# Performance work log

Measured on AMD Instinct MI355X. Metric: run time of the kernel, lower is better.

The kernel has to match this reference:

```python
import jax, jax.numpy as jnp
import numpy as np

B, N, C, T, K = 32, 4096, 768, 1000, 20

def setup_inputs() -> dict:
    key = jax.random.key(0)
    k1, k2, k3, k4 = jax.random.split(key, 4)
    g_feat = jax.random.normal(k1, (B, 1, C), dtype=jnp.float32)
    inp = jax.random.normal(k2, (B, N, C), dtype=jnp.float32)
    tau = jax.random.uniform(k3, (1,), dtype=jnp.float32)
    text_embeddings = jax.random.normal(k4, (T, C), dtype=jnp.float32) * 0.01
    return {"g_feat": g_feat, "input": inp, "tau": tau, "text_embeddings": text_embeddings}


def reference(g_feat, input, tau, text_embeddings):
    feat = input  # [B, N, C]
    # 1x1 conv of global feature against text embeddings -> class logits [B, T]
    vg_logit = jnp.einsum('bc,tc->bt', g_feat[:, 0, :], text_embeddings)
    # top-20 candidate categories per image
    _, indices = jax.lax.top_k(vg_logit, K)              # [B, K]
    agg_text_features = text_embeddings[indices]          # [B, K, C] gather
    # per-pixel logits against the 20 gathered text embeddings
    seg_logit = jnp.exp(tau[0]) * jnp.einsum('bkc,bnc->bkn', agg_text_features, feat)  # [B, K, N]
    # hard (straight-through) softmax over candidate axis (dim=-2)
    y_soft = jax.nn.softmax(seg_logit, axis=-2)
    idx = jnp.argmax(seg_logit, axis=-2)                  # [B, N]
    y_hard = jnp.moveaxis(jax.nn.one_hot(idx, K, dtype=seg_logit.dtype), -1, -2)  # [B, K, N]
    attn = y_hard - jax.lax.stop_gradient(y_soft) + y_soft
    # normalize over pixel axis (assign_eps = 1.0)
    assign_attn = attn / (jnp.sum(attn, axis=-1, keepdims=True) + 1.0)
    # combine: [B, N, K] @ [B, K, C] -> [B, N, C]
    text_grids = jnp.einsum('bkn,bkc->bnc', assign_attn, agg_text_features)
    return text_grids
```

## Files before the change

### kernel.cpp

```cpp
#include <hip/hip_runtime.h>
#include <cfloat>

#define B_ 32
#define N_ 4096
#define C_ 768
#define T_ 1000
#define K_ 20

#define PXB 256
#define PHC 16
#define NPH (C_/PHC)
#define GAP_TH 1e-3f
#define MAXF 16384

typedef float f32x4 __attribute__((ext_vector_type(4)));

__global__ __launch_bounds__(256) void k1_logits(const float* __restrict__ g_feat,
                                                 const float* __restrict__ text,
                                                 double* __restrict__ logits,
                                                 int* __restrict__ cnt,
                                                 int* __restrict__ flagcnt) {
    int b = blockIdx.x;
    int wid = threadIdx.x >> 6, lane = threadIdx.x & 63;
    int t = blockIdx.y * 4 + wid;
    if (b == 0 && blockIdx.y == 0) {
        for (int i = threadIdx.x; i < B_ * K_; i += 256) cnt[i] = 0;
        if (threadIdx.x == 0) flagcnt[0] = 0;
    }
    const float* g = g_feat + b * C_;
    const float* e = text + t * C_;
    double s = 0.0;
    #pragma unroll
    for (int j = 0; j < 12; ++j) {
        int c = lane + 64 * j;
        s += (double)g[c] * (double)e[c];
    }
    #pragma unroll
    for (int m = 32; m; m >>= 1) s += __shfl_xor(s, m);
    if (lane == 0) logits[b * T_ + t] = s;
}

__global__ __launch_bounds__(256) void k1b_topk(const double* __restrict__ logits,
                                                const float* __restrict__ text,
                                                float* __restrict__ agg,
                                                int* __restrict__ sel) {
    __shared__ int ssel[K_];
    int b = blockIdx.x, tid = threadIdx.x, lane = tid & 63;
    if (tid < 64) {
        double v[16];
        #pragma unroll
        for (int j = 0; j < 16; ++j) {
            int t = lane + 64 * j;
            v[j] = (t < T_) ? logits[b * T_ + t] : -DBL_MAX;
        }
        for (int it = 0; it < K_; ++it) {
            double bv = -DBL_MAX; int bi = 0x7fffffff;
            #pragma unroll
            for (int j = 0; j < 16; ++j) {
                int t = lane + 64 * j;
                if (v[j] > bv) { bv = v[j]; bi = t; }
            }
            #pragma unroll
            for (int m = 32; m; m >>= 1) {
                double ov = __shfl_xor(bv, m); int oi = __shfl_xor(bi, m);
                if (ov > bv || (ov == bv && oi < bi)) { bv = ov; bi = oi; }
            }
            if (lane == 0) ssel[it] = bi;
            #pragma unroll
            for (int j = 0; j < 16; ++j) {
                int t = lane + 64 * j;
                if (t == bi) v[j] = -DBL_MAX;
            }
        }
    }
    __syncthreads();
    if (tid < K_) sel[b * K_ + tid] = ssel[tid];
    for (int i = tid; i < K_ * C_; i += 256) {
        int j = i / C_, c = i - j * C_;
        agg[b * K_ * C_ + i] = text[ssel[j] * C_ + c];
    }
}

__global__ __launch_bounds__(128) void k2_argmax(const float* __restrict__ feat,
                                                 const float* __restrict__ agg,
                                                 int* __restrict__ kidx,
                                                 int* __restrict__ cnt,
                                                 int* __restrict__ flagcnt,
                                                 int* __restrict__ flaglist) {
    __shared__ float fbuf[3][PXB * PHC];
    __shared__ float ebuf[3][512];
    __shared__ int scnt[K_];
    int bx = blockIdx.x;
    int b = bx >> 4, tile = bx & 15;
    int n0 = tile * PXB;
    int tid = threadIdx.x, wid = tid >> 6, lane = tid & 63;
    if (tid < K_) scnt[tid] = 0;
    __syncthreads();

    const float* fb = feat + ((size_t)b * N_ + n0) * C_;
    const float* eb = agg + b * (K_ * C_);

    int se = wid * 64 + lane;
    int ce = se < 80 ? se : 79;
    const float* esrc = eb + (ce >> 2) * C_ + (ce & 3) * 4;

    auto stage = [&](int p, int bufi) {
        #pragma unroll
        for (int ii = 0; ii < 8; ++ii) {
            int s = (wid * 8 + ii) * 64 + lane;
            int c = s ^ ((s >> 3) & 7);
            int px = c >> 2, j = c & 3;
            const float* g = fb + (size_t)px * C_ + p * PHC + j * 4;
            float* d = &fbuf[bufi][(wid * 8 + ii) * 256];
            __builtin_amdgcn_global_load_lds((const __attribute__((address_space(1))) void*)g,
                                             (__attribute__((address_space(3))) void*)d, 16, 0, 0);
        }
        {
            const float* g = esrc + p * PHC;
            float* d = &ebuf[bufi][wid * 256];
            __builtin_amdgcn_global_load_lds((const __attribute__((address_space(1))) void*)g,
                                             (__attribute__((address_space(3))) void*)d, 16, 0, 0);
        }
    };

    float acc0[K_], acc1[K_];
    #pragma unroll
    for (int k = 0; k < K_; ++k) { acc0[k] = 0.f; acc1[k] = 0.f; }

    stage(0, 0);
    stage(1, 1);

    int p0 = tid, p1 = tid + 128;
    #pragma unroll 1
    for (int p = 0; p < NPH; ++p) {
        int bufi = p % 3;
        if (p + 2 < NPH) {
            stage(p + 2, (p + 2) % 3);
            asm volatile("s_waitcnt vmcnt(18)" ::: "memory");
        } else if (p + 1 < NPH) {
            asm volatile("s_waitcnt vmcnt(9)" ::: "memory");
        } else {
            asm volatile("s_waitcnt vmcnt(0)" ::: "memory");
        }
        asm volatile("s_barrier" ::: "memory");

        const float* fB = fbuf[bufi];
        const float* eB = ebuf[bufi];
        f32x4 F0[4], F1[4];
        #pragma unroll
        for (int j = 0; j < 4; ++j) {
            int c0 = p0 * 4 + j, h0 = c0 ^ ((c0 >> 3) & 7);
            F0[j] = *(const f32x4*)(fB + h0 * 4);
            int c1 = p1 * 4 + j, h1 = c1 ^ ((c1 >> 3) & 7);
            F1[j] = *(const f32x4*)(fB + h1 * 4);
        }
        #pragma unroll
        for (int k = 0; k < K_; ++k) {
            float a0 = acc0[k], a1 = acc1[k];
            #pragma unroll
            for (int j = 0; j < 4; ++j) {
                f32x4 e = *(const f32x4*)(eB + (k * 4 + j) * 4);
                a0 = fmaf(F0[j].x, e.x, a0); a0 = fmaf(F0[j].y, e.y, a0);
                a0 = fmaf(F0[j].z, e.z, a0); a0 = fmaf(F0[j].w, e.w, a0);
                a1 = fmaf(F1[j].x, e.x, a1); a1 = fmaf(F1[j].y, e.y, a1);
                a1 = fmaf(F1[j].z, e.z, a1); a1 = fmaf(F1[j].w, e.w, a1);
            }
            acc0[k] = a0; acc1[k] = a1;
        }
        asm volatile("s_barrier" ::: "memory");
    }

    #pragma unroll
    for (int q = 0; q < 2; ++q) {
        float* acc = q ? acc1 : acc0;
        float m1 = acc[0]; int i1 = 0; float m2 = -FLT_MAX;
        #pragma unroll
        for (int k = 1; k < K_; ++k) {
            float v = acc[k];
            if (v > m1) { m2 = m1; m1 = v; i1 = k; }
            else if (v > m2) m2 = v;
        }
        int n = n0 + tid + q * 128;
        kidx[b * N_ + n] = i1;
        atomicAdd(&scnt[i1], 1);
        if (m1 - m2 < GAP_TH) {
            int pos = atomicAdd(flagcnt, 1);
            if (pos < MAXF) flaglist[pos] = b * N_ + n;
        }
    }
    __syncthreads();
    if (tid < K_) atomicAdd(&cnt[b * K_ + tid], scnt[tid]);
}

__global__ __launch_bounds__(256) void k25_refine(const float* __restrict__ feat,
                                                  const float* __restrict__ agg,
                                                  int* __restrict__ kidx,
                                                  int* __restrict__ cnt,
                                                  const int* __restrict__ flagcnt,
                                                  const int* __restrict__ flaglist) {
    int wid = threadIdx.x >> 6, lane = threadIdx.x & 63;
    int wg = blockIdx.x * 4 + wid;
    int nf = flagcnt[0]; if (nf > MAXF) nf = MAXF;
    for (int e = wg; e < nf; e += gridDim.x * 4) {
        int pix = flaglist[e];
        int b = pix >> 12;
        const float* fr = feat + (size_t)pix * C_;
        const float* ebase = agg + b * K_ * C_;
        double fd[12];
        #pragma unroll
        for (int j = 0; j < 12; ++j) fd[j] = (double)fr[lane + 64 * j];
        double best = -DBL_MAX; int bi = 0;
        for (int k = 0; k < K_; ++k) {
            const float* er = ebase + k * C_;
            double s = 0.0;
            #pragma unroll
            for (int j = 0; j < 12; ++j) s += fd[j] * (double)er[lane + 64 * j];
            #pragma unroll
            for (int m = 32; m; m >>= 1) s += __shfl_xor(s, m);
            if (s > best) { best = s; bi = k; }
        }
        if (lane == 0) {
            int old = kidx[pix];
            if (old != bi) {
                kidx[pix] = bi;
                atomicSub(&cnt[b * K_ + old], 1);
                atomicAdd(&cnt[b * K_ + bi], 1);
            }
        }
    }
}

__global__ __launch_bounds__(256) void k4_out(const float* __restrict__ agg,
                                              const int* __restrict__ cnt,
                                              const int* __restrict__ kidx,
                                              float* __restrict__ out) {
    int wid = threadIdx.x >> 6, lane = threadIdx.x & 63;
    int wg = blockIdx.x * 4 + wid;
    int base = wg * 8;
    int b = base >> 12;
    int kk[8];
    #pragma unroll
    for (int i = 0; i < 8; ++i) kk[i] = kidx[base + i];
    float sc[8];
    #pragma unroll
    for (int i = 0; i < 8; ++i) sc[i] = 1.0f / ((float)cnt[b * K_ + kk[i]] + 1.0f);
    const f32x4* agg4 = (const f32x4*)agg;
    f32x4* out4 = (f32x4*)out;
    #pragma unroll
    for (int i = 0; i < 8; ++i) {
        const f32x4* a4 = agg4 + (size_t)(b * K_ + kk[i]) * (C_ / 4);
        f32x4* o4 = out4 + (size_t)(base + i) * (C_ / 4);
        #pragma unroll
        for (int j = 0; j < 3; ++j) {
            f32x4 v = a4[lane + 64 * j];
            v *= sc[i];
            __builtin_nontemporal_store(v, &o4[lane + 64 * j]);
        }
    }
}

extern "C" void kernel_launch(void* const* d_in, const int* in_sizes, int n_in,
                              void* d_out, int out_size, void* d_ws, size_t ws_size,
                              hipStream_t stream) {
    const float* g_feat = (const float*)d_in[0];
    const float* feat   = (const float*)d_in[1];
    const float* text   = (const float*)d_in[3];
    float* out = (float*)d_out;

    char* ws = (char*)d_ws;
    double* logits = (double*)(ws + 0);
    float*  agg    = (float*) (ws + 262144);
    int*    sel    = (int*)   (ws + 2228224);
    int*    cnt    = (int*)   (ws + 2230784);
    int*    flagc  = (int*)   (ws + 2233344);
    int*    flagl  = (int*)   (ws + 2233408);
    int*    kidx   = (int*)   (ws + 2301504);

    k1_logits<<<dim3(32, 250), 256, 0, stream>>>(g_feat, text, logits, cnt, flagc);
    k1b_topk<<<32, 256, 0, stream>>>(logits, text, agg, sel);
    k2_argmax<<<32 * 16, 128, 0, stream>>>(feat, agg, kidx, cnt, flagc, flagl);
    k25_refine<<<64, 256, 0, stream>>>(feat, agg, kidx, cnt, flagc, flagl);
    k4_out<<<4096, 256, 0, stream>>>(agg, cnt, kidx, out);
}
```

Before: 299.6 us.

## Compute per-pixel logits with split-bf16 MFMA instead of fp32 FMA

Replaces the scalar fp32 FMA dot product in the argmax kernel with MFMA 16x16x32 bf16 instructions. Each fp32 operand is split into a hi and a lo bf16 part, and three cross products are accumulated to keep near-fp32 accuracy. Features are loaded into registers, converted and written to swizzled LDS; the text embeddings are pre-split into bf16 hi/lo tables in the top-k kernel. It also lowers the gap threshold for the fp32 refine pass, widens the refine grid and switches the output stores from nontemporal to regular. The risk is borderline argmax mismatches if the split-bf16 error exceeds the tighter threshold.

```diff
diff --git a/kernel.cpp b/kernel.cpp
--- a/kernel.cpp
+++ b/kernel.cpp
@@ -8,12 +8,19 @@
 #define K_ 20
 
 #define PXB 256
-#define PHC 16
+#define PHC 32
 #define NPH (C_/PHC)
-#define GAP_TH 1e-3f
+#define GAP_TH 1e-4f
 #define MAXF 16384
 
 typedef float f32x4 __attribute__((ext_vector_type(4)));
+typedef int   i32x4 __attribute__((ext_vector_type(4)));
+typedef short s16x8 __attribute__((ext_vector_type(8)));
+
+__device__ __forceinline__ unsigned short bf_rne(float x) {
+    unsigned u = __float_as_uint(x);
+    return (unsigned short)((u + 0x7fffu + ((u >> 16) & 1u)) >> 16);
+}
 
 __global__ __launch_bounds__(256) void k1_logits(const float* __restrict__ g_feat,
                                                  const float* __restrict__ text,
@@ -43,7 +50,8 @@
 __global__ __launch_bounds__(256) void k1b_topk(const double* __restrict__ logits,
                                                 const float* __restrict__ text,
                                                 float* __restrict__ agg,
-                                                int* __restrict__ sel) {
+                                                unsigned short* __restrict__ Ehi,
+                                                unsigned short* __restrict__ Elo) {
     __shared__ int ssel[K_];
     int b = blockIdx.x, tid = threadIdx.x, lane = tid & 63;
     if (tid < 64) {
@@ -74,21 +82,29 @@
         }
     }
     __syncthreads();
-    if (tid < K_) sel[b * K_ + tid] = ssel[tid];
     for (int i = tid; i < K_ * C_; i += 256) {
         int j = i / C_, c = i - j * C_;
         agg[b * K_ * C_ + i] = text[ssel[j] * C_ + c];
     }
-}
-
-__global__ __launch_bounds__(128) void k2_argmax(const float* __restrict__ feat,
-                                                 const float* __restrict__ agg,
-                                                 int* __restrict__ kidx,
-                                                 int* __restrict__ cnt,
-                                                 int* __restrict__ flagcnt,
-                                                 int* __restrict__ flaglist) {
-    __shared__ float fbuf[3][PXB * PHC];
-    __shared__ float ebuf[3][512];
+    for (int i = tid; i < 32 * C_; i += 256) {
+        int r = i / C_, c = i - r * C_;
+        float v = (r < K_) ? text[ssel[r] * C_ + c] : 0.f;
+        unsigned u = __float_as_uint(v);
+        float fh = __uint_as_float(u & 0xffff0000u);
+        Ehi[(size_t)b * 32 * C_ + i] = (unsigned short)(u >> 16);
+        Elo[(size_t)b * 32 * C_ + i] = bf_rne(v - fh);
+    }
+}
+
+__global__ __launch_bounds__(256, 2) void k2_argmax(const float* __restrict__ feat,
+                                                    const unsigned short* __restrict__ Ehi,
+                                                    const unsigned short* __restrict__ Elo,
+                                                    int* __restrict__ kidx,
+                                                    int* __restrict__ cnt,
+                                                    int* __restrict__ flagcnt,
+                                                    int* __restrict__ flaglist) {
+    __shared__ unsigned short hiT[2][PXB * PHC];
+    __shared__ unsigned short loT[2][PXB * PHC];
     __shared__ int scnt[K_];
     int bx = blockIdx.x;
     int b = bx >> 4, tile = bx & 15;
@@ -98,94 +114,120 @@
     __syncthreads();
 
     const float* fb = feat + ((size_t)b * N_ + n0) * C_;
-    const float* eb = agg + b * (K_ * C_);
-
-    int se = wid * 64 + lane;
-    int ce = se < 80 ? se : 79;
-    const float* esrc = eb + (ce >> 2) * C_ + (ce & 3) * 4;
-
-    auto stage = [&](int p, int bufi) {
-        #pragma unroll
-        for (int ii = 0; ii < 8; ++ii) {
-            int s = (wid * 8 + ii) * 64 + lane;
-            int c = s ^ ((s >> 3) & 7);
-            int px = c >> 2, j = c & 3;
-            const float* g = fb + (size_t)px * C_ + p * PHC + j * 4;
-            float* d = &fbuf[bufi][(wid * 8 + ii) * 256];
-            __builtin_amdgcn_global_load_lds((const __attribute__((address_space(1))) void*)g,
-                                             (__attribute__((address_space(3))) void*)d, 16, 0, 0);
-        }
-        {
-            const float* g = esrc + p * PHC;
-            float* d = &ebuf[bufi][wid * 256];
-            __builtin_amdgcn_global_load_lds((const __attribute__((address_space(1))) void*)g,
-                                             (__attribute__((address_space(3))) void*)d, 16, 0, 0);
-        }
+    const unsigned short* Eh = Ehi + (size_t)b * 32 * C_;
+    const unsigned short* El = Elo + (size_t)b * 32 * C_;
+    int r2 = (tid >> 1) & 3;
+    int arow = lane & 15, acg = lane >> 4;
+
+    f32x4 fr[8];
+    auto LOADF = [&](int p) {
+        const f32x4* fp_ = (const f32x4*)(fb + (size_t)tid * C_ + p * PHC);
+        #pragma unroll
+        for (int q = 0; q < 8; ++q) fr[q] = fp_[q ^ (2 * r2)];
     };
-
-    float acc0[K_], acc1[K_];
-    #pragma unroll
-    for (int k = 0; k < K_; ++k) { acc0[k] = 0.f; acc1[k] = 0.f; }
-
-    stage(0, 0);
-    stage(1, 1);
-
-    int p0 = tid, p1 = tid + 128;
+    auto CVTW = [&](int buf) {
+        #pragma unroll
+        for (int j = 0; j < 4; ++j) {
+            unsigned hu[8], lu[8];
+            #pragma unroll
+            for (int m = 0; m < 8; ++m) {
+                float x = (m < 4) ? fr[2 * j][m] : fr[2 * j + 1][m - 4];
+                unsigned u = __float_as_uint(x);
+                float fh = __uint_as_float(u & 0xffff0000u);
+                hu[m] = u >> 16;
+                lu[m] = bf_rne(x - fh);
+            }
+            int slot = tid * 4 + (j ^ r2);
+            i32x4 hv = { (int)(hu[0] | (hu[1] << 16)), (int)(hu[2] | (hu[3] << 16)),
+                         (int)(hu[4] | (hu[5] << 16)), (int)(hu[6] | (hu[7] << 16)) };
+            i32x4 lv = { (int)(lu[0] | (lu[1] << 16)), (int)(lu[2] | (lu[3] << 16)),
+                         (int)(lu[4] | (lu[5] << 16)), (int)(lu[6] | (lu[7] << 16)) };
+            *(i32x4*)&hiT[buf][slot * 8] = hv;
+            *(i32x4*)&loT[buf][slot * 8] = lv;
+        }
+    };
+
+    s16x8 Ach0, Ach1, Acl0, Acl1, Anh0, Anh1, Anl0, Anl1;
+    auto LOADA = [&](int p, s16x8& h0, s16x8& h1, s16x8& l0, s16x8& l1) {
+        int co = p * PHC + acg * 8;
+        h0 = *(const s16x8*)(Eh + (size_t)arow * C_ + co);
+        h1 = *(const s16x8*)(Eh + (size_t)(16 + arow) * C_ + co);
+        l0 = *(const s16x8*)(El + (size_t)arow * C_ + co);
+        l1 = *(const s16x8*)(El + (size_t)(16 + arow) * C_ + co);
+    };
+
+    f32x4 acc0[4], acc1[4];
+    #pragma unroll
+    for (int i = 0; i < 4; ++i) { acc0[i] = (f32x4)0.f; acc1[i] = (f32x4)0.f; }
+
+    LOADF(0);
+    CVTW(0);
+    LOADF(1);
+    LOADA(0, Ach0, Ach1, Acl0, Acl1);
+    LOADA(1, Anh0, Anh1, Anl0, Anl1);
+    __syncthreads();
+
     #pragma unroll 1
     for (int p = 0; p < NPH; ++p) {
-        int bufi = p % 3;
-        if (p + 2 < NPH) {
-            stage(p + 2, (p + 2) % 3);
-            asm volatile("s_waitcnt vmcnt(18)" ::: "memory");
-        } else if (p + 1 < NPH) {
-            asm volatile("s_waitcnt vmcnt(9)" ::: "memory");
-        } else {
-            asm volatile("s_waitcnt vmcnt(0)" ::: "memory");
+        int cur = p & 1;
+        if (p + 1 < NPH) {
+            CVTW(cur ^ 1);
+            if (p + 2 < NPH) LOADF(p + 2);
+            asm volatile("s_waitcnt lgkmcnt(0)" ::: "memory");
         }
         asm volatile("s_barrier" ::: "memory");
 
-        const float* fB = fbuf[bufi];
-        const float* eB = ebuf[bufi];
-        f32x4 F0[4], F1[4];
-        #pragma unroll
-        for (int j = 0; j < 4; ++j) {
-            int c0 = p0 * 4 + j, h0 = c0 ^ ((c0 >> 3) & 7);
-            F0[j] = *(const f32x4*)(fB + h0 * 4);
-            int c1 = p1 * 4 + j, h1 = c1 ^ ((c1 >> 3) & 7);
-            F1[j] = *(const f32x4*)(fB + h1 * 4);
-        }
-        #pragma unroll
-        for (int k = 0; k < K_; ++k) {
-            float a0 = acc0[k], a1 = acc1[k];
-            #pragma unroll
-            for (int j = 0; j < 4; ++j) {
-                f32x4 e = *(const f32x4*)(eB + (k * 4 + j) * 4);
-                a0 = fmaf(F0[j].x, e.x, a0); a0 = fmaf(F0[j].y, e.y, a0);
-                a0 = fmaf(F0[j].z, e.z, a0); a0 = fmaf(F0[j].w, e.w, a0);
-                a1 = fmaf(F1[j].x, e.x, a1); a1 = fmaf(F1[j].y, e.y, a1);
-                a1 = fmaf(F1[j].z, e.z, a1); a1 = fmaf(F1[j].w, e.w, a1);
-            }
-            acc0[k] = a0; acc1[k] = a1;
+        #pragma unroll
+        for (int i = 0; i < 4; ++i) {
+            int slot = (wid * 64 + i * 16 + arow) * 4 + acg;
+            s16x8 Bh = *(const s16x8*)&hiT[cur][slot * 8];
+            s16x8 Bl = *(const s16x8*)&loT[cur][slot * 8];
+            acc0[i] = __builtin_amdgcn_mfma_f32_16x16x32_bf16(Ach0, Bh, acc0[i], 0, 0, 0);
+            acc1[i] = __builtin_amdgcn_mfma_f32_16x16x32_bf16(Ach1, Bh, acc1[i], 0, 0, 0);
+            acc0[i] = __builtin_amdgcn_mfma_f32_16x16x32_bf16(Ach0, Bl, acc0[i], 0, 0, 0);
+            acc1[i] = __builtin_amdgcn_mfma_f32_16x16x32_bf16(Ach1, Bl, acc1[i], 0, 0, 0);
+            acc0[i] = __builtin_amdgcn_mfma_f32_16x16x32_bf16(Acl0, Bh, acc0[i], 0, 0, 0);
+            acc1[i] = __builtin_amdgcn_mfma_f32_16x16x32_bf16(Acl1, Bh, acc1[i], 0, 0, 0);
         }
         asm volatile("s_barrier" ::: "memory");
-    }
-
-    #pragma unroll
-    for (int q = 0; q < 2; ++q) {
-        float* acc = q ? acc1 : acc0;
-        float m1 = acc[0]; int i1 = 0; float m2 = -FLT_MAX;
-        #pragma unroll
-        for (int k = 1; k < K_; ++k) {
-            float v = acc[k];
-            if (v > m1) { m2 = m1; m1 = v; i1 = k; }
+
+        Ach0 = Anh0; Ach1 = Anh1; Acl0 = Anl0; Acl1 = Anl1;
+        if (p + 2 < NPH) LOADA(p + 2, Anh0, Anh1, Anl0, Anl1);
+    }
+
+    #pragma unroll
+    for (int i = 0; i < 4; ++i) {
+        int kb = acg * 4;
+        float m1 = acc0[i][0]; int i1 = kb; float m2 = -FLT_MAX;
+        #pragma unroll
+        for (int r = 1; r < 4; ++r) {
+            float v = acc0[i][r];
+            if (v > m1) { m2 = m1; m1 = v; i1 = kb + r; }
             else if (v > m2) m2 = v;
         }
-        int n = n0 + tid + q * 128;
-        kidx[b * N_ + n] = i1;
-        atomicAdd(&scnt[i1], 1);
-        if (m1 - m2 < GAP_TH) {
-            int pos = atomicAdd(flagcnt, 1);
-            if (pos < MAXF) flaglist[pos] = b * N_ + n;
+        if (acg == 0) {
+            #pragma unroll
+            for (int r = 0; r < 4; ++r) {
+                float v = acc1[i][r];
+                if (v > m1) { m2 = m1; m1 = v; i1 = 16 + r; }
+                else if (v > m2) m2 = v;
+            }
+        }
+        #pragma unroll
+        for (int s = 16; s < 64; s <<= 1) {
+            float om1 = __shfl_xor(m1, s); int oi1 = __shfl_xor(i1, s);
+            float om2 = __shfl_xor(m2, s);
+            if (om1 > m1 || (om1 == m1 && oi1 < i1)) { m2 = fmaxf(m1, om2); m1 = om1; i1 = oi1; }
+            else { m2 = fmaxf(m2, om1); }
+        }
+        if (lane < 16) {
+            int n = n0 + wid * 64 + i * 16 + lane;
+            kidx[b * N_ + n] = i1;
+            atomicAdd(&scnt[i1], 1);
+            if (m1 - m2 < GAP_TH) {
+                int pos = atomicAdd(flagcnt, 1);
+                if (pos < MAXF) flaglist[pos] = b * N_ + n;
+            }
         }
     }
     __syncthreads();
@@ -254,7 +296,7 @@
         for (int j = 0; j < 3; ++j) {
             f32x4 v = a4[lane + 64 * j];
             v *= sc[i];
-            __builtin_nontemporal_store(v, &o4[lane + 64 * j]);
+            o4[lane + 64 * j] = v;
         }
     }
 }
@@ -268,17 +310,18 @@
     float* out = (float*)d_out;
 
     char* ws = (char*)d_ws;
-    double* logits = (double*)(ws + 0);
-    float*  agg    = (float*) (ws + 262144);
-    int*    sel    = (int*)   (ws + 2228224);
-    int*    cnt    = (int*)   (ws + 2230784);
-    int*    flagc  = (int*)   (ws + 2233344);
-    int*    flagl  = (int*)   (ws + 2233408);
-    int*    kidx   = (int*)   (ws + 2301504);
+    double* logits        = (double*)(ws + 0);
+    float*  agg           = (float*) (ws + 262144);
+    int*    cnt           = (int*)   (ws + 2230784);
+    int*    flagc         = (int*)   (ws + 2233344);
+    int*    flagl         = (int*)   (ws + 2233408);
+    int*    kidx          = (int*)   (ws + 2301504);
+    unsigned short* Ehi   = (unsigned short*)(ws + 2825792);
+    unsigned short* Elo   = (unsigned short*)(ws + 4398656);
 
     k1_logits<<<dim3(32, 250), 256, 0, stream>>>(g_feat, text, logits, cnt, flagc);
-    k1b_topk<<<32, 256, 0, stream>>>(logits, text, agg, sel);
-    k2_argmax<<<32 * 16, 128, 0, stream>>>(feat, agg, kidx, cnt, flagc, flagl);
-    k25_refine<<<64, 256, 0, stream>>>(feat, agg, kidx, cnt, flagc, flagl);
+    k1b_topk<<<32, 256, 0, stream>>>(logits, text, agg, Ehi, Elo);
+    k2_argmax<<<32 * 16, 256, 0, stream>>>(feat, Ehi, Elo, kidx, cnt, flagc, flagl);
+    k25_refine<<<1024, 256, 0, stream>>>(feat, agg, kidx, cnt, flagc, flagl);
     k4_out<<<4096, 256, 0, stream>>>(agg, cnt, kidx, out);
 }
```

New measurement: 273.5 us. 8.7% less time.
